# Kernel tuning notes

Measured on AMD Instinct MI355X. Metric: run time of the kernel, lower is better.

## Reference

```python
import jax, jax.numpy as jnp
import numpy as np

N, L, H, D = 4, 1024, 8, 64

def setup_inputs() -> dict:
    key = jax.random.key(0)
    ks = jax.random.split(key, 6)
    names = ["q_real", "q_imag", "k_real", "k_imag", "v_real", "v_imag"]
    return {n: jax.random.normal(k, (N, L, H, D), dtype=jnp.float32) for n, k in zip(names, ks)}


def reference(q_real, q_imag, k_real, k_imag, v_real, v_imag):
    d = q_real.shape[-1]
    scale = 1.0 / np.sqrt(d).astype(np.float32)
    # complex QK^T: (ar+i*ai)(br+i*bi) -> 4 real einsums, scores shape (N,H,L,S)
    s_real = (jnp.einsum('nlhd,nshd->nhls', q_real, k_real)
              - jnp.einsum('nlhd,nshd->nhls', q_imag, k_imag))
    s_imag = (jnp.einsum('nlhd,nshd->nhls', q_real, k_imag)
              + jnp.einsum('nlhd,nshd->nhls', q_imag, k_real))
    # complex softmax = independent softmax on real and imag parts
    w_real = jax.nn.softmax(scale * s_real, axis=-1)
    w_imag = jax.nn.softmax(scale * s_imag, axis=-1)
    # complex_dropout on complex input is identity (original code drops nothing)
    # complex AV
    u_real = (jnp.einsum('nhls,nshd->nlhd', w_real, v_real)
              - jnp.einsum('nhls,nshd->nlhd', w_imag, v_imag))
    u_imag = (jnp.einsum('nhls,nshd->nlhd', w_real, v_imag)
              + jnp.einsum('nhls,nshd->nlhd', w_imag, v_real))
    # attn_weights.permute(0,2,1,3).mean(dim=-2): (N,H,L,S)->(N,L,H,S), mean over H -> (N,L,S)
    a_real = w_real.mean(axis=1)
    a_imag = w_imag.mean(axis=1)
    return (u_real, u_imag, a_real, a_imag)
```

## Files before the change

### kernel.cpp

```cpp
#include <hip/hip_runtime.h>

#define N_ 4
#define L_ 1024
#define H_ 8
#define D_ 64

typedef _Float16 f16x8 __attribute__((ext_vector_type(8)));
typedef float f32x4 __attribute__((ext_vector_type(4)));

#define MFMA(A, B, C) __builtin_amdgcn_mfma_f32_16x16x32_f16(A, B, C, 0, 0, 0)

__device__ __forceinline__ ushort f2h(float x) {
    union { _Float16 h; ushort u; } c;
    c.h = (_Float16)x;
    return c.u;
}
__device__ __forceinline__ f16x8 ld8(const ushort* p) {
    return *(const f16x8*)p;
}
__device__ __forceinline__ f16x8 negf(f16x8 a) {
    uint4 u = __builtin_bit_cast(uint4, a);
    u.x ^= 0x80008000u; u.y ^= 0x80008000u; u.z ^= 0x80008000u; u.w ^= 0x80008000u;
    return __builtin_bit_cast(f16x8, u);
}
__device__ __forceinline__ f16x8 cvt8s(const float* p, float s) {
    float4 a = *(const float4*)p;
    float4 b = *(const float4*)(p + 4);
    union { f16x8 v; _Float16 e[8]; } u;
    u.e[0] = (_Float16)(a.x * s); u.e[1] = (_Float16)(a.y * s);
    u.e[2] = (_Float16)(a.z * s); u.e[3] = (_Float16)(a.w * s);
    u.e[4] = (_Float16)(b.x * s); u.e[5] = (_Float16)(b.y * s);
    u.e[6] = (_Float16)(b.z * s); u.e[7] = (_Float16)(b.w * s);
    return u.v;
}
#define SCQ 0.18033688011112f
__device__ __forceinline__ f16x8 cvt8(const float* p) { return cvt8s(p, SCQ); }

__device__ __forceinline__ void gl_lds16(const ushort* g, ushort* l) {
    __builtin_amdgcn_global_load_lds(
        (const __attribute__((address_space(1))) unsigned int*)g,
        (__attribute__((address_space(3))) unsigned int*)l, 16, 0, 0);
}

__global__ void cvt_k(const float* __restrict__ k_r, const float* __restrict__ k_i,
                      ushort* __restrict__ dst) {
    int gid = blockIdx.x * 256 + threadIdx.x;
    int aid = gid >> 19;
    int idx = (gid & 0x7FFFF) << 2;
    int d  = idx & 63;
    int l  = (idx >> 6) & 1023;
    int hh = (idx >> 16) & 7;
    int n  = idx >> 19;
    const float* src = aid ? k_i : k_r;
    const float4 v = *(const float4*)(src + (((long)n * 1024 + l) * 8 + hh) * 64 + d);
    ushort4 o = make_ushort4(f2h(v.x), f2h(v.y), f2h(v.z), f2h(v.w));
    *(ushort4*)(dst + ((long)aid << 21) + idx) = o;
}

__global__ void cvt_v(const float* __restrict__ vr, const float* __restrict__ vi,
                      ushort* __restrict__ dst) {
    __shared__ ushort t[64][72];
    int bid = blockIdx.x;
    int aid = bid >> 9;
    int b   = bid & 511;
    int s0  = (b & 15) << 6;
    int hh  = (b >> 4) & 7;
    int n   = b >> 7;
    const float* src = aid ? vi : vr;
    int tid = threadIdx.x;
    int r  = tid >> 4;
    int cq = (tid & 15) << 2;
#pragma unroll
    for (int it = 0; it < 4; ++it) {
        int s = s0 + it * 16 + r;
        const float4 v = *(const float4*)(src + (((long)n * 1024 + s) * 8 + hh) * 64 + cq);
        t[it * 16 + r][cq + 0] = f2h(v.x);
        t[it * 16 + r][cq + 1] = f2h(v.y);
        t[it * 16 + r][cq + 2] = f2h(v.z);
        t[it * 16 + r][cq + 3] = f2h(v.w);
    }
    __syncthreads();
#pragma unroll
    for (int it = 0; it < 4; ++it) {
        int dd = it * 16 + r;
        ushort4 o;
        o.x = t[cq + 0][dd]; o.y = t[cq + 1][dd]; o.z = t[cq + 2][dd]; o.w = t[cq + 3][dd];
        *(ushort4*)(dst + ((long)aid << 21) + (((long)n * 8 + hh) * 64 + dd) * 1024 + s0 + cq) = o;
    }
}

#define BFLY(x)                                                             \
    x += __shfl_xor(x, 1); x += __shfl_xor(x, 2);                           \
    x += __shfl_xor(x, 4); x += __shfl_xor(x, 8);


__launch_bounds__(512, 2)
__global__ void attn_u(const float* __restrict__ qr_g, const float* __restrict__ qi_g,
                       const ushort* __restrict__ ws, float* __restrict__ rdbuf,
                       float* __restrict__ out) {
    __shared__ ushort stgK[2][2][32][64];
    __shared__ ushort stgV[2][2][64][32];
    __shared__ ushort wtl[8][2][16][32];

    const int tid  = threadIdx.x;
    const int lane = tid & 63;
    const int wv   = tid >> 6;
    const int col  = lane & 15;
    const int g    = lane >> 4;

    const int id = blockIdx.x;
    const int x  = id & 7;
    const int j  = id >> 3;
    const int nh = x * 4 + (j >> 3);
    const int n  = nh >> 3;
    const int h  = nh & 7;
    const int l0 = (j & 7) * 128 + wv * 16;

    const ushort* Kr = ws + ((long)nh << 16);
    const ushort* Ki = ws + (1l << 21) + ((long)nh << 16);
    const ushort* Vr = ws + (2l << 21) + ((long)nh << 16);
    const ushort* Vi = ws + (3l << 21) + ((long)nh << 16);

    const long qg = (((long)n * 1024 + l0 + col) * 8 + h) * 64 + g * 8;
    const f16x8 qr0 = cvt8(qr_g + qg), qr1 = cvt8(qr_g + qg + 32);
    const f16x8 qi0 = cvt8(qi_g + qg), qi1 = cvt8(qi_g + qg + 32);
    const f16x8 qn0 = negf(qi0), qn1 = negf(qi1);

    const int sp  = wv >> 2;
    const int krow = (wv & 3) * 8 + (lane >> 3);
    const int kbs  = ((lane & 7) ^ (krow & 7)) * 8;
    const int vrow = (wv & 3) * 16 + (lane >> 2);
    const int vbs  = ((lane & 3) ^ (vrow & 3)) * 8;
    const ushort* Kst = sp ? Ki : Kr;
    const ushort* Vst = sp ? Vi : Vr;

    float dRs[4] = {0.f, 0.f, 0.f, 0.f};
    float dIs[4] = {0.f, 0.f, 0.f, 0.f};
    f32x4 uRR[4], uII[4], uRI[4], uIR[4];
#pragma unroll
    for (int db = 0; db < 4; ++db) {
        uRR[db] = (f32x4){0.f, 0.f, 0.f, 0.f};
        uII[db] = (f32x4){0.f, 0.f, 0.f, 0.f};
        uRI[db] = (f32x4){0.f, 0.f, 0.f, 0.f};
        uIR[db] = (f32x4){0.f, 0.f, 0.f, 0.f};
    }

    const int kx  = (g ^ (col & 7)) * 8;
    const int kx2 = ((g + 4) ^ (col & 7)) * 8;
    const int vx  = (g ^ (col & 3)) * 8;

#define STAGE(buf, cc)                                                       \
    do {                                                                     \
        gl_lds16(Kst + (long)((cc) * 32 + krow) * 64 + kbs,                  \
                 &stgK[buf][sp][(wv & 3) * 8][0]);                           \
        gl_lds16(Vst + (long)vrow * 1024 + (cc) * 32 + vbs,                  \
                 &stgV[buf][sp][(wv & 3) * 16][0]);                          \
    } while (0)

    STAGE(0, 0);
    __syncthreads();

    for (int cc = 0; cc < 32; ++cc) {
        const int buf = cc & 1;
        if (cc < 31) STAGE(buf ^ 1, cc + 1);

#pragma unroll
        for (int sb = 0; sb < 2; ++sb) {
            const int row = sb * 16 + col;
            f16x8 kr0 = ld8(&stgK[buf][0][row][kx]);
            f16x8 kr1 = ld8(&stgK[buf][0][row][kx2]);
            f16x8 ki0 = ld8(&stgK[buf][1][row][kx]);
            f16x8 ki1 = ld8(&stgK[buf][1][row][kx2]);
            f32x4 a0 = (f32x4){0.f, 0.f, 0.f, 0.f};
            a0 = MFMA(qr0, kr0, a0); a0 = MFMA(qr1, kr1, a0);
            a0 = MFMA(qn0, ki0, a0); a0 = MFMA(qn1, ki1, a0);
            f32x4 a1 = (f32x4){0.f, 0.f, 0.f, 0.f};
            a1 = MFMA(qr0, ki0, a1); a1 = MFMA(qr1, ki1, a1);
            a1 = MFMA(qi0, kr0, a1); a1 = MFMA(qi1, kr1, a1);
#pragma unroll
            for (int r = 0; r < 4; ++r) {
                const float wf = exp2f(a0[r]);
                const float vf = exp2f(a1[r]);
                dRs[r] += wf;
                dIs[r] += vf;
                const int l = 4 * g + r;
                const int scol = sb * 16 + col;
                const int us = l * 32 + (((scol >> 3) ^ (l & 3)) << 3) + (scol & 7);
                (&wtl[wv][0][0][0])[us] = f2h(wf);
                (&wtl[wv][1][0][0])[us] = f2h(vf);
            }
        }

        f16x8 wr0 = ld8(&wtl[wv][0][col][vx]);
        f16x8 wi0 = ld8(&wtl[wv][1][col][vx]);
#pragma unroll
        for (int db = 0; db < 4; ++db) {
            const int row = db * 16 + col;
            f16x8 vr0 = ld8(&stgV[buf][0][row][vx]);
            f16x8 vi0 = ld8(&stgV[buf][1][row][vx]);
            uRR[db] = MFMA(wr0, vr0, uRR[db]);
            uII[db] = MFMA(wi0, vi0, uII[db]);
            uRI[db] = MFMA(wr0, vi0, uRI[db]);
            uIR[db] = MFMA(wi0, vr0, uIR[db]);
        }

        __syncthreads();
    }

    BFLY(dRs[0]) BFLY(dRs[1]) BFLY(dRs[2]) BFLY(dRs[3])
    BFLY(dIs[0]) BFLY(dIs[1]) BFLY(dIs[2]) BFLY(dIs[3])

    float rdR[4], rdI[4];
#pragma unroll
    for (int r = 0; r < 4; ++r) { rdR[r] = 1.f / dRs[r]; rdI[r] = 1.f / dIs[r]; }

    if (col == 0) {
#pragma unroll
        for (int r = 0; r < 4; ++r) {
            rdbuf[nh * 1024 + l0 + 4 * g + r] = rdR[r];
            rdbuf[32768 + nh * 1024 + l0 + 4 * g + r] = rdI[r];
        }
    }

    const long OFF_UI = 2097152;
#pragma unroll
    for (int db = 0; db < 4; ++db) {
#pragma unroll
        for (int r = 0; r < 4; ++r) {
            const int l = l0 + 4 * g + r;
            const int d = db * 16 + col;
            const long base = (((long)n * L_ + l) * H_ + h) * D_ + d;
            out[base] = uRR[db][r] * rdR[r] - uII[db][r] * rdI[r];
            out[OFF_UI + base] = uRI[db][r] * rdR[r] + uIR[db][r] * rdI[r];
        }
    }
#undef STAGE
}

__launch_bounds__(256, 4)
__global__ void kern_a(const float* __restrict__ qr_g, const float* __restrict__ qi_g,
                       const ushort* __restrict__ ws, const float* __restrict__ rdbuf,
                       float* __restrict__ out) {
    __shared__ ushort stgK[2][2][64][64];
    __shared__ float lrd[8][2][64];

    const int tid  = threadIdx.x;
    const int lane = tid & 63;
    const int wv   = tid >> 6;
    const int col  = lane & 15;
    const int g    = lane >> 4;

    const int id  = blockIdx.x;
    const int x   = id & 7;
    const int q   = id >> 3;
    const int n   = x >> 1;
    const int idx = (x & 1) * 128 + q;
    const int lt0 = (idx >> 4) * 64;
    const int sc  = idx & 15;
    const int l0  = lt0 + wv * 16;

    const ushort* KrB = ws + ((long)(n * 8) << 16);
    const ushort* KiB = ws + (1l << 21) + ((long)(n * 8) << 16);

#pragma unroll
    for (int i = 0; i < 4; ++i) {
        const int t = i * 256 + tid;
        (&lrd[0][0][0])[t] =
            rdbuf[((t >> 6) & 1) * 32768 + (n * 8 + (t >> 7)) * 1024 + lt0 + (t & 63)];
    }

    const int sp   = wv >> 1;
    const int kbs  = ((lane & 7) ^ (lane >> 3)) * 8;

#define STAGEA(buf, hh)                                                      \
    do {                                                                     \
        const ushort* Kp = (sp ? KiB : KrB) + ((long)(hh) << 16);            \
        _Pragma("unroll")                                                    \
        for (int i = 0; i < 4; ++i) {                                        \
            const int krow = (wv & 1) * 32 + i * 8 + (lane >> 3);            \
            gl_lds16(Kp + (long)(sc * 64 + krow) * 64 + kbs,                 \
                     &stgK[buf][sp][(wv & 1) * 32 + i * 8][0]);              \
        }                                                                    \
    } while (0)

    f32x4 aR[4], aI[4];
#pragma unroll
    for (int i = 0; i < 4; ++i) {
        aR[i] = (f32x4){0.f, 0.f, 0.f, 0.f};
        aI[i] = (f32x4){0.f, 0.f, 0.f, 0.f};
    }

    const int kx  = (g ^ (col & 7)) * 8;
    const int kx2 = ((g + 4) ^ (col & 7)) * 8;

    STAGEA(0, 0);
    __syncthreads();

    for (int h = 0; h < 8; ++h) {
        const int buf = h & 1;
        if (h < 7) STAGEA(buf ^ 1, h + 1);

        const long qg = (((long)n * 1024 + l0 + col) * 8 + h) * 64 + g * 8;
        const f16x8 qr0 = cvt8(qr_g + qg), qr1 = cvt8(qr_g + qg + 32);
        const f16x8 qi0 = cvt8(qi_g + qg), qi1 = cvt8(qi_g + qg + 32);
        const f16x8 qn0 = negf(qi0), qn1 = negf(qi1);

        float rdR[4], rdI[4];
#pragma unroll
        for (int r = 0; r < 4; ++r) {
            rdR[r] = lrd[h][0][wv * 16 + 4 * g + r];
            rdI[r] = lrd[h][1][wv * 16 + 4 * g + r];
        }

#pragma unroll
        for (int sb = 0; sb < 4; ++sb) {
            const int row = sb * 16 + col;
            f16x8 kr0 = ld8(&stgK[buf][0][row][kx]);
            f16x8 kr1 = ld8(&stgK[buf][0][row][kx2]);
            f16x8 ki0 = ld8(&stgK[buf][1][row][kx]);
            f16x8 ki1 = ld8(&stgK[buf][1][row][kx2]);
            f32x4 a0 = (f32x4){0.f, 0.f, 0.f, 0.f};
            a0 = MFMA(qr0, kr0, a0); a0 = MFMA(qr1, kr1, a0);
            a0 = MFMA(qn0, ki0, a0); a0 = MFMA(qn1, ki1, a0);
            f32x4 a1 = (f32x4){0.f, 0.f, 0.f, 0.f};
            a1 = MFMA(qr0, ki0, a1); a1 = MFMA(qr1, ki1, a1);
            a1 = MFMA(qi0, kr0, a1); a1 = MFMA(qi1, kr1, a1);
#pragma unroll
            for (int r = 0; r < 4; ++r) {
                aR[sb][r] += exp2f(a0[r]) * rdR[r];
                aI[sb][r] += exp2f(a1[r]) * rdI[r];
            }
        }
        __syncthreads();
    }

    const long OFF_AR = 4194304;
    const long OFF_AI = 8388608;
#pragma unroll
    for (int sb = 0; sb < 4; ++sb) {
#pragma unroll
        for (int r = 0; r < 4; ++r) {
            const int l = l0 + 4 * g + r;
            const int s = sc * 64 + sb * 16 + col;
            const long ab = ((long)n * 1024 + l) * 1024 + s;
            out[OFF_AR + ab] = aR[sb][r] * 0.125f;
            out[OFF_AI + ab] = aI[sb][r] * 0.125f;
        }
    }
#undef STAGEA
}

extern "C" void kernel_launch(void* const* d_in, const int* in_sizes, int n_in,
                              void* d_out, int out_size, void* d_ws, size_t ws_size,
                              hipStream_t stream) {
    const float* qr = (const float*)d_in[0];
    const float* qi = (const float*)d_in[1];
    const float* kr = (const float*)d_in[2];
    const float* ki = (const float*)d_in[3];
    const float* vr = (const float*)d_in[4];
    const float* vi = (const float*)d_in[5];
    ushort* ws = (ushort*)d_ws;
    float* rdbuf = (float*)((char*)d_ws + (16ull << 20));
    float* out = (float*)d_out;

    hipLaunchKernelGGL(cvt_k, dim3(4096), dim3(256), 0, stream, kr, ki, ws);
    hipLaunchKernelGGL(cvt_v, dim3(1024), dim3(256), 0, stream, vr, vi, ws + (2l << 21));
    hipLaunchKernelGGL(attn_u, dim3(256), dim3(512), 0, stream, qr, qi, ws, rdbuf, out);
    hipLaunchKernelGGL(kern_a, dim3(1024), dim3(256), 0, stream, qr, qi, ws, rdbuf, out);
}
```

Before: 111.9 us.

## Split attn_u key range across two wave halves and combine partials in LDS

attn_u now launches 512 blocks of 64 query rows instead of 256 blocks of 128 rows. Within each block, two groups of four waves each process half of the key sequence (16 chunks each rather than 32). The partial softmax denominators and unnormalized outputs are combined through shared memory before the store. This doubles the grid to fill more CUs and halves the serial loop length, at the cost of more K/V staging traffic per block, extra LDS, several added barriers and a higher occupancy target in launch_bounds.

```diff
diff --git a/kernel.cpp b/kernel.cpp
--- a/kernel.cpp
+++ b/kernel.cpp
@@ -94,27 +94,29 @@
     x += __shfl_xor(x, 4); x += __shfl_xor(x, 8);
 
 
-__launch_bounds__(512, 2)
+__launch_bounds__(512, 4)
 __global__ void attn_u(const float* __restrict__ qr_g, const float* __restrict__ qi_g,
                        const ushort* __restrict__ ws, float* __restrict__ rdbuf,
                        float* __restrict__ out) {
-    __shared__ ushort stgK[2][2][32][64];
-    __shared__ ushort stgV[2][2][64][32];
+    __shared__ ushort stgK[2][2][2][32][64];
+    __shared__ ushort stgV[2][2][2][64][32];
     __shared__ ushort wtl[8][2][16][32];
 
     const int tid  = threadIdx.x;
     const int lane = tid & 63;
     const int wv   = tid >> 6;
+    const int sh   = wv >> 2;
+    const int lsub = wv & 3;
     const int col  = lane & 15;
     const int g    = lane >> 4;
 
     const int id = blockIdx.x;
     const int x  = id & 7;
     const int j  = id >> 3;
-    const int nh = x * 4 + (j >> 3);
+    const int nh = x * 4 + (j >> 4);
     const int n  = nh >> 3;
     const int h  = nh & 7;
-    const int l0 = (j & 7) * 128 + wv * 16;
+    const int l0 = (j & 15) * 64 + lsub * 16;
 
     const ushort* Kr = ws + ((long)nh << 16);
     const ushort* Ki = ws + (1l << 21) + ((long)nh << 16);
@@ -126,13 +128,12 @@
     const f16x8 qi0 = cvt8(qi_g + qg), qi1 = cvt8(qi_g + qg + 32);
     const f16x8 qn0 = negf(qi0), qn1 = negf(qi1);
 
-    const int sp  = wv >> 2;
-    const int krow = (wv & 3) * 8 + (lane >> 3);
-    const int kbs  = ((lane & 7) ^ (krow & 7)) * 8;
-    const int vrow = (wv & 3) * 16 + (lane >> 2);
-    const int vbs  = ((lane & 3) ^ (vrow & 3)) * 8;
-    const ushort* Kst = sp ? Ki : Kr;
-    const ushort* Vst = sp ? Vi : Vr;
+    const int kp  = lsub >> 1;
+    const int hf  = lsub & 1;
+    const int kbs = ((lane & 7) ^ (lane >> 3)) * 8;
+    const int vbs = (((lane & 3) ^ ((lane >> 2) & 3) ^ g) & 3) * 8;
+    const ushort* Kst = kp ? Ki : Kr;
+    const ushort* Vst = kp ? Vi : Vr;
 
     float dRs[4] = {0.f, 0.f, 0.f, 0.f};
     float dIs[4] = {0.f, 0.f, 0.f, 0.f};
@@ -147,30 +148,35 @@
 
     const int kx  = (g ^ (col & 7)) * 8;
     const int kx2 = ((g + 4) ^ (col & 7)) * 8;
-    const int vx  = (g ^ (col & 3)) * 8;
+    const int vx  = ((g ^ (col & 3) ^ ((col >> 2) & 3)) & 3) * 8;
 
 #define STAGE(buf, cc)                                                       \
     do {                                                                     \
-        gl_lds16(Kst + (long)((cc) * 32 + krow) * 64 + kbs,                  \
-                 &stgK[buf][sp][(wv & 3) * 8][0]);                           \
-        gl_lds16(Vst + (long)vrow * 1024 + (cc) * 32 + vbs,                  \
-                 &stgV[buf][sp][(wv & 3) * 16][0]);                          \
+        const int csh = sh * 16 + (cc);                                      \
+        gl_lds16(Kst + (long)(csh * 32 + hf * 16 + (lane >> 3)) * 64 + kbs,  \
+                 &stgK[buf][sh][kp][hf * 16][0]);                            \
+        gl_lds16(Kst + (long)(csh * 32 + hf * 16 + 8 + (lane >> 3)) * 64 + kbs, \
+                 &stgK[buf][sh][kp][hf * 16 + 8][0]);                        \
+        gl_lds16(Vst + (long)(hf * 32 + (lane >> 2)) * 1024 + csh * 32 + vbs, \
+                 &stgV[buf][sh][kp][hf * 32][0]);                            \
+        gl_lds16(Vst + (long)(hf * 32 + 16 + (lane >> 2)) * 1024 + csh * 32 + vbs, \
+                 &stgV[buf][sh][kp][hf * 32 + 16][0]);                       \
     } while (0)
 
     STAGE(0, 0);
     __syncthreads();
 
-    for (int cc = 0; cc < 32; ++cc) {
+    for (int cc = 0; cc < 16; ++cc) {
         const int buf = cc & 1;
-        if (cc < 31) STAGE(buf ^ 1, cc + 1);
+        if (cc < 15) STAGE(buf ^ 1, cc + 1);
 
 #pragma unroll
         for (int sb = 0; sb < 2; ++sb) {
             const int row = sb * 16 + col;
-            f16x8 kr0 = ld8(&stgK[buf][0][row][kx]);
-            f16x8 kr1 = ld8(&stgK[buf][0][row][kx2]);
-            f16x8 ki0 = ld8(&stgK[buf][1][row][kx]);
-            f16x8 ki1 = ld8(&stgK[buf][1][row][kx2]);
+            f16x8 kr0 = ld8(&stgK[buf][sh][0][row][kx]);
+            f16x8 kr1 = ld8(&stgK[buf][sh][0][row][kx2]);
+            f16x8 ki0 = ld8(&stgK[buf][sh][1][row][kx]);
+            f16x8 ki1 = ld8(&stgK[buf][sh][1][row][kx2]);
             f32x4 a0 = (f32x4){0.f, 0.f, 0.f, 0.f};
             a0 = MFMA(qr0, kr0, a0); a0 = MFMA(qr1, kr1, a0);
             a0 = MFMA(qn0, ki0, a0); a0 = MFMA(qn1, ki1, a0);
@@ -185,7 +191,8 @@
                 dIs[r] += vf;
                 const int l = 4 * g + r;
                 const int scol = sb * 16 + col;
-                const int us = l * 32 + (((scol >> 3) ^ (l & 3)) << 3) + (scol & 7);
+                const int pos = ((scol >> 3) ^ r ^ g) & 3;
+                const int us = l * 32 + pos * 8 + (scol & 7);
                 (&wtl[wv][0][0][0])[us] = f2h(wf);
                 (&wtl[wv][1][0][0])[us] = f2h(vf);
             }
@@ -196,8 +203,8 @@
 #pragma unroll
         for (int db = 0; db < 4; ++db) {
             const int row = db * 16 + col;
-            f16x8 vr0 = ld8(&stgV[buf][0][row][vx]);
-            f16x8 vi0 = ld8(&stgV[buf][1][row][vx]);
+            f16x8 vr0 = ld8(&stgV[buf][sh][0][row][vx]);
+            f16x8 vi0 = ld8(&stgV[buf][sh][1][row][vx]);
             uRR[db] = MFMA(wr0, vr0, uRR[db]);
             uII[db] = MFMA(wi0, vi0, uII[db]);
             uRI[db] = MFMA(wr0, vi0, uRI[db]);
@@ -210,11 +217,27 @@
     BFLY(dRs[0]) BFLY(dRs[1]) BFLY(dRs[2]) BFLY(dRs[3])
     BFLY(dIs[0]) BFLY(dIs[1]) BFLY(dIs[2]) BFLY(dIs[3])
 
+    float* sstf = (float*)&wtl[0][0][0][0];
+    if (col == 0) {
+#pragma unroll
+        for (int r = 0; r < 4; ++r) {
+            sstf[((sh * 4 + lsub) * 2 + 0) * 16 + 4 * g + r] = dRs[r];
+            sstf[((sh * 4 + lsub) * 2 + 1) * 16 + 4 * g + r] = dIs[r];
+        }
+    }
+    __syncthreads();
+
     float rdR[4], rdI[4];
 #pragma unroll
-    for (int r = 0; r < 4; ++r) { rdR[r] = 1.f / dRs[r]; rdI[r] = 1.f / dIs[r]; }
-
-    if (col == 0) {
+    for (int r = 0; r < 4; ++r) {
+        const int row = 4 * g + r;
+        rdR[r] = 1.f / (sstf[(lsub * 2 + 0) * 16 + row] +
+                        sstf[((4 + lsub) * 2 + 0) * 16 + row]);
+        rdI[r] = 1.f / (sstf[(lsub * 2 + 1) * 16 + row] +
+                        sstf[((4 + lsub) * 2 + 1) * 16 + row]);
+    }
+
+    if (sh == 0 && col == 0) {
 #pragma unroll
         for (int r = 0; r < 4; ++r) {
             rdbuf[nh * 1024 + l0 + 4 * g + r] = rdR[r];
@@ -222,16 +245,47 @@
         }
     }
 
-    const long OFF_UI = 2097152;
+    f32x4 oR[4], oI[4];
 #pragma unroll
     for (int db = 0; db < 4; ++db) {
 #pragma unroll
         for (int r = 0; r < 4; ++r) {
-            const int l = l0 + 4 * g + r;
-            const int d = db * 16 + col;
-            const long base = (((long)n * L_ + l) * H_ + h) * D_ + d;
-            out[base] = uRR[db][r] * rdR[r] - uII[db][r] * rdI[r];
-            out[OFF_UI + base] = uRI[db][r] * rdR[r] + uIR[db][r] * rdI[r];
+            oR[db][r] = uRR[db][r] * rdR[r] - uII[db][r] * rdI[r];
+            oI[db][r] = uRI[db][r] * rdR[r] + uIR[db][r] * rdI[r];
+        }
+    }
+    __syncthreads();
+
+    float* cb = (float*)&wtl[lsub * 2][0][0][0];
+    if (sh == 1) {
+#pragma unroll
+        for (int db = 0; db < 4; ++db) *(f32x4*)&cb[lane * 16 + db * 4] = oR[db];
+    }
+    __syncthreads();
+    if (sh == 0) {
+#pragma unroll
+        for (int db = 0; db < 4; ++db) oR[db] += *(f32x4*)&cb[lane * 16 + db * 4];
+    }
+    __syncthreads();
+    if (sh == 1) {
+#pragma unroll
+        for (int db = 0; db < 4; ++db) *(f32x4*)&cb[lane * 16 + db * 4] = oI[db];
+    }
+    __syncthreads();
+
+    if (sh == 0) {
+        const long OFF_UI = 2097152;
+#pragma unroll
+        for (int db = 0; db < 4; ++db) {
+            f32x4 oid = oI[db] + *(f32x4*)&cb[lane * 16 + db * 4];
+#pragma unroll
+            for (int r = 0; r < 4; ++r) {
+                const int l = l0 + 4 * g + r;
+                const int d = db * 16 + col;
+                const long base = (((long)n * L_ + l) * H_ + h) * D_ + d;
+                out[base] = oR[db][r];
+                out[OFF_UI + base] = oid[r];
+            }
         }
     }
 #undef STAGE
@@ -365,6 +419,6 @@
 
     hipLaunchKernelGGL(cvt_k, dim3(4096), dim3(256), 0, stream, kr, ki, ws);
     hipLaunchKernelGGL(cvt_v, dim3(1024), dim3(256), 0, stream, vr, vi, ws + (2l << 21));
-    hipLaunchKernelGGL(attn_u, dim3(256), dim3(512), 0, stream, qr, qi, ws, rdbuf, out);
+    hipLaunchKernelGGL(attn_u, dim3(512), dim3(512), 0, stream, qr, qi, ws, rdbuf, out);
     hipLaunchKernelGGL(kern_a, dim3(1024), dim3(256), 0, stream, qr, qi, ws, rdbuf, out);
 }
```

Result: slower. 194.5 us (+73.8%).

## Split real and imaginary softmax paths across wave halves, doubling the grid

Applied to the files above, without the earlier changes.

Each 512-thread block now covers 64 query rows instead of 128. The first four waves compute the real score path and the last four compute the imaginary path, so each wave does half the QK MFMAs, half the exp work and half the AV accumulators. The real and imaginary partial outputs are combined through LDS, reusing the K staging buffer, with extra barriers. The grid doubles to 512 blocks and launch bounds ask for 4 blocks per CU. This aims for more parallelism and less register pressure, at the cost of staging each K/V tile for twice as many blocks and adding an LDS reduction step.

```diff
diff --git a/kernel.cpp b/kernel.cpp
--- a/kernel.cpp
+++ b/kernel.cpp
@@ -94,27 +94,29 @@
     x += __shfl_xor(x, 4); x += __shfl_xor(x, 8);
 
 
-__launch_bounds__(512, 2)
+__launch_bounds__(512, 4)
 __global__ void attn_u(const float* __restrict__ qr_g, const float* __restrict__ qi_g,
                        const ushort* __restrict__ ws, float* __restrict__ rdbuf,
                        float* __restrict__ out) {
     __shared__ ushort stgK[2][2][32][64];
     __shared__ ushort stgV[2][2][64][32];
-    __shared__ ushort wtl[8][2][16][32];
+    __shared__ ushort wtl[8][16][32];
 
     const int tid  = threadIdx.x;
     const int lane = tid & 63;
     const int wv   = tid >> 6;
+    const int p    = wv >> 2;
+    const int lsub = wv & 3;
     const int col  = lane & 15;
     const int g    = lane >> 4;
 
     const int id = blockIdx.x;
     const int x  = id & 7;
     const int j  = id >> 3;
-    const int nh = x * 4 + (j >> 3);
+    const int nh = x * 4 + (j >> 4);
     const int n  = nh >> 3;
     const int h  = nh & 7;
-    const int l0 = (j & 7) * 128 + wv * 16;
+    const int l0 = (j & 15) * 64 + lsub * 16;
 
     const ushort* Kr = ws + ((long)nh << 16);
     const ushort* Ki = ws + (1l << 21) + ((long)nh << 16);
@@ -122,27 +124,23 @@
     const ushort* Vi = ws + (3l << 21) + ((long)nh << 16);
 
     const long qg = (((long)n * 1024 + l0 + col) * 8 + h) * 64 + g * 8;
+    const float sgn = p ? SCQ : -SCQ;
     const f16x8 qr0 = cvt8(qr_g + qg), qr1 = cvt8(qr_g + qg + 32);
-    const f16x8 qi0 = cvt8(qi_g + qg), qi1 = cvt8(qi_g + qg + 32);
-    const f16x8 qn0 = negf(qi0), qn1 = negf(qi1);
-
-    const int sp  = wv >> 2;
-    const int krow = (wv & 3) * 8 + (lane >> 3);
+    const f16x8 qx0 = cvt8s(qi_g + qg, sgn), qx1 = cvt8s(qi_g + qg + 32, sgn);
+
+    const int krow = lsub * 8 + (lane >> 3);
     const int kbs  = ((lane & 7) ^ (krow & 7)) * 8;
-    const int vrow = (wv & 3) * 16 + (lane >> 2);
+    const int vrow = lsub * 16 + (lane >> 2);
     const int vbs  = ((lane & 3) ^ (vrow & 3)) * 8;
-    const ushort* Kst = sp ? Ki : Kr;
-    const ushort* Vst = sp ? Vi : Vr;
-
-    float dRs[4] = {0.f, 0.f, 0.f, 0.f};
-    float dIs[4] = {0.f, 0.f, 0.f, 0.f};
-    f32x4 uRR[4], uII[4], uRI[4], uIR[4];
+    const ushort* Kst = p ? Ki : Kr;
+    const ushort* Vst = p ? Vi : Vr;
+
+    float ds[4] = {0.f, 0.f, 0.f, 0.f};
+    f32x4 uA[4], uB[4];
 #pragma unroll
     for (int db = 0; db < 4; ++db) {
-        uRR[db] = (f32x4){0.f, 0.f, 0.f, 0.f};
-        uII[db] = (f32x4){0.f, 0.f, 0.f, 0.f};
-        uRI[db] = (f32x4){0.f, 0.f, 0.f, 0.f};
-        uIR[db] = (f32x4){0.f, 0.f, 0.f, 0.f};
+        uA[db] = (f32x4){0.f, 0.f, 0.f, 0.f};
+        uB[db] = (f32x4){0.f, 0.f, 0.f, 0.f};
     }
 
     const int kx  = (g ^ (col & 7)) * 8;
@@ -152,9 +150,9 @@
 #define STAGE(buf, cc)                                                       \
     do {                                                                     \
         gl_lds16(Kst + (long)((cc) * 32 + krow) * 64 + kbs,                  \
-                 &stgK[buf][sp][(wv & 3) * 8][0]);                           \
+                 &stgK[buf][p][lsub * 8][0]);                                \
         gl_lds16(Vst + (long)vrow * 1024 + (cc) * 32 + vbs,                  \
-                 &stgV[buf][sp][(wv & 3) * 16][0]);                          \
+                 &stgV[buf][p][lsub * 16][0]);                               \
     } while (0)
 
     STAGE(0, 0);
@@ -167,71 +165,90 @@
 #pragma unroll
         for (int sb = 0; sb < 2; ++sb) {
             const int row = sb * 16 + col;
-            f16x8 kr0 = ld8(&stgK[buf][0][row][kx]);
-            f16x8 kr1 = ld8(&stgK[buf][0][row][kx2]);
-            f16x8 ki0 = ld8(&stgK[buf][1][row][kx]);
-            f16x8 ki1 = ld8(&stgK[buf][1][row][kx2]);
+            f16x8 ka0 = ld8(&stgK[buf][p][row][kx]);
+            f16x8 ka1 = ld8(&stgK[buf][p][row][kx2]);
+            f16x8 kb0 = ld8(&stgK[buf][p ^ 1][row][kx]);
+            f16x8 kb1 = ld8(&stgK[buf][p ^ 1][row][kx2]);
             f32x4 a0 = (f32x4){0.f, 0.f, 0.f, 0.f};
-            a0 = MFMA(qr0, kr0, a0); a0 = MFMA(qr1, kr1, a0);
-            a0 = MFMA(qn0, ki0, a0); a0 = MFMA(qn1, ki1, a0);
-            f32x4 a1 = (f32x4){0.f, 0.f, 0.f, 0.f};
-            a1 = MFMA(qr0, ki0, a1); a1 = MFMA(qr1, ki1, a1);
-            a1 = MFMA(qi0, kr0, a1); a1 = MFMA(qi1, kr1, a1);
+            a0 = MFMA(qr0, ka0, a0); a0 = MFMA(qr1, ka1, a0);
+            a0 = MFMA(qx0, kb0, a0); a0 = MFMA(qx1, kb1, a0);
 #pragma unroll
             for (int r = 0; r < 4; ++r) {
                 const float wf = exp2f(a0[r]);
-                const float vf = exp2f(a1[r]);
-                dRs[r] += wf;
-                dIs[r] += vf;
+                ds[r] += wf;
                 const int l = 4 * g + r;
                 const int scol = sb * 16 + col;
                 const int us = l * 32 + (((scol >> 3) ^ (l & 3)) << 3) + (scol & 7);
-                (&wtl[wv][0][0][0])[us] = f2h(wf);
-                (&wtl[wv][1][0][0])[us] = f2h(vf);
+                (&wtl[wv][0][0])[us] = f2h(wf);
             }
         }
 
-        f16x8 wr0 = ld8(&wtl[wv][0][col][vx]);
-        f16x8 wi0 = ld8(&wtl[wv][1][col][vx]);
+        f16x8 w0 = ld8(&wtl[wv][col][vx]);
 #pragma unroll
         for (int db = 0; db < 4; ++db) {
             const int row = db * 16 + col;
             f16x8 vr0 = ld8(&stgV[buf][0][row][vx]);
             f16x8 vi0 = ld8(&stgV[buf][1][row][vx]);
-            uRR[db] = MFMA(wr0, vr0, uRR[db]);
-            uII[db] = MFMA(wi0, vi0, uII[db]);
-            uRI[db] = MFMA(wr0, vi0, uRI[db]);
-            uIR[db] = MFMA(wi0, vr0, uIR[db]);
+            uA[db] = MFMA(w0, vr0, uA[db]);
+            uB[db] = MFMA(w0, vi0, uB[db]);
         }
 
         __syncthreads();
     }
 
-    BFLY(dRs[0]) BFLY(dRs[1]) BFLY(dRs[2]) BFLY(dRs[3])
-    BFLY(dIs[0]) BFLY(dIs[1]) BFLY(dIs[2]) BFLY(dIs[3])
-
-    float rdR[4], rdI[4];
-#pragma unroll
-    for (int r = 0; r < 4; ++r) { rdR[r] = 1.f / dRs[r]; rdI[r] = 1.f / dIs[r]; }
+    BFLY(ds[0]) BFLY(ds[1]) BFLY(ds[2]) BFLY(ds[3])
+
+    float rd[4];
+#pragma unroll
+    for (int r = 0; r < 4; ++r) rd[r] = 1.f / ds[r];
 
     if (col == 0) {
 #pragma unroll
+        for (int r = 0; r < 4; ++r)
+            rdbuf[p * 32768 + nh * 1024 + l0 + 4 * g + r] = rd[r];
+    }
+
+#pragma unroll
+    for (int db = 0; db < 4; ++db) {
+#pragma unroll
         for (int r = 0; r < 4; ++r) {
-            rdbuf[nh * 1024 + l0 + 4 * g + r] = rdR[r];
-            rdbuf[32768 + nh * 1024 + l0 + 4 * g + r] = rdI[r];
-        }
-    }
-
-    const long OFF_UI = 2097152;
-#pragma unroll
-    for (int db = 0; db < 4; ++db) {
-#pragma unroll
-        for (int r = 0; r < 4; ++r) {
-            const int l = l0 + 4 * g + r;
-            const int d = db * 16 + col;
-            const long base = (((long)n * L_ + l) * H_ + h) * D_ + d;
-            out[base] = uRR[db][r] * rdR[r] - uII[db][r] * rdI[r];
-            out[OFF_UI + base] = uRI[db][r] * rdR[r] + uIR[db][r] * rdI[r];
+            uA[db][r] *= rd[r];
+            uB[db][r] *= rd[r];
+        }
+    }
+
+    float* cb = (float*)&stgK[0][0][0][0];
+    const int ci = (lsub * 64 + lane) * 16;
+    if (p == 1) {
+#pragma unroll
+        for (int db = 0; db < 4; ++db) *(f32x4*)&cb[ci + db * 4] = uB[db];
+    }
+    __syncthreads();
+    f32x4 oR[4];
+    if (p == 0) {
+#pragma unroll
+        for (int db = 0; db < 4; ++db) oR[db] = uA[db] - *(f32x4*)&cb[ci + db * 4];
+    }
+    __syncthreads();
+    if (p == 1) {
+#pragma unroll
+        for (int db = 0; db < 4; ++db) *(f32x4*)&cb[ci + db * 4] = uA[db];
+    }
+    __syncthreads();
+
+    if (p == 0) {
+        const long OFF_UI = 2097152;
+#pragma unroll
+        for (int db = 0; db < 4; ++db) {
+            f32x4 oI = uB[db] + *(f32x4*)&cb[ci + db * 4];
+#pragma unroll
+            for (int r = 0; r < 4; ++r) {
+                const int l = l0 + 4 * g + r;
+                const int d = db * 16 + col;
+                const long base = (((long)n * L_ + l) * H_ + h) * D_ + d;
+                out[base] = oR[db][r];
+                out[OFF_UI + base] = oI[r];
+            }
         }
     }
 #undef STAGE
@@ -365,6 +382,6 @@
 
     hipLaunchKernelGGL(cvt_k, dim3(4096), dim3(256), 0, stream, kr, ki, ws);
     hipLaunchKernelGGL(cvt_v, dim3(1024), dim3(256), 0, stream, vr, vi, ws + (2l << 21));
-    hipLaunchKernelGGL(attn_u, dim3(256), dim3(512), 0, stream, qr, qi, ws, rdbuf, out);
+    hipLaunchKernelGGL(attn_u, dim3(512), dim3(512), 0, stream, qr, qi, ws, rdbuf, out);
     hipLaunchKernelGGL(kern_a, dim3(1024), dim3(256), 0, stream, qr, qi, ws, rdbuf, out);
 }
```

Result: slower. 116.5 us (+4.1%).
